# Kernel tuning notes

Measured on AMD Instinct MI355X. Metric: run time of the kernel, lower is better.

Reference implementation:

```python
import jax, jax.numpy as jnp
import numpy as np

H = 51  # n_hidden
B = 8192  # batch
T = 2048  # seq_len
FUTURE = 64


def setup_inputs() -> dict:
    key = jax.random.key(0)
    ks = jax.random.split(key, 12)
    s = 1.0 / np.sqrt(H)
    u = lambda k, shape: jax.random.uniform(k, shape, jnp.float32, -s, s)
    return {
        "x": jax.random.normal(ks[0], (B, T), jnp.float32),
        "W_ih1": u(ks[1], (4 * H, 1)),
        "W_hh1": u(ks[2], (4 * H, H)),
        "b_ih1": u(ks[3], (4 * H,)),
        "b_hh1": u(ks[4], (4 * H,)),
        "W_ih2": u(ks[5], (4 * H, H)),
        "W_hh2": u(ks[6], (4 * H, H)),
        "b_ih2": u(ks[7], (4 * H,)),
        "b_hh2": u(ks[8], (4 * H,)),
        "W_out": u(ks[9], (1, H)),
        "b_out": u(ks[10], (1,)),
        "future": FUTURE,
    }


def _lstm_cell(x, h, c, Wih, Whh, bih, bhh):
    # PyTorch LSTMCell: gates ordered i, f, g, o
    g = x @ Wih.T + h @ Whh.T + (bih + bhh)  # [B, 4H]
    i, f, gg, o = jnp.split(g, 4, axis=-1)
    i = jax.nn.sigmoid(i)
    f = jax.nn.sigmoid(f)
    gg = jnp.tanh(gg)
    o = jax.nn.sigmoid(o)
    c2 = f * c + i * gg
    h2 = o * jnp.tanh(c2)
    return h2, c2


def reference(x, W_ih1, W_hh1, b_ih1, b_hh1, W_ih2, W_hh2, b_ih2, b_hh2,
              W_out, b_out, future):
    Bn = x.shape[0]
    h1 = jnp.zeros((Bn, H), x.dtype)
    c1 = jnp.zeros((Bn, H), x.dtype)

    def emit(h1, c1):
        # Quirk of the original code: layer-2 state is layer-1's CURRENT (h1, c1),
        # and layer-2's own state is never carried forward.
        h2, _ = _lstm_cell(h1, h1, c1, W_ih2, W_hh2, b_ih2, b_hh2)
        return h2 @ W_out.T + b_out  # [B, 1]

    def step(carry, xt):
        h1, c1 = carry
        h1, c1 = _lstm_cell(xt, h1, c1, W_ih1, W_hh1, b_ih1, b_hh1)
        out = emit(h1, c1)
        return (h1, c1), out

    xs = jnp.swapaxes(x, 0, 1)[:, :, None]  # [T, B, 1]
    (h1, c1), outs = jax.lax.scan(step, (h1, c1), xs)
    outs = outs[..., 0].T  # [B, T]

    def fstep(carry, _):
        h1, c1, out = carry
        h1, c1 = _lstm_cell(out, h1, c1, W_ih1, W_hh1, b_ih1, b_hh1)
        out = emit(h1, c1)
        return (h1, c1, out), out

    last = outs[:, -1:]
    _, fouts = jax.lax.scan(fstep, (h1, c1, last), None, length=future)
    fouts = fouts[..., 0].T if future > 0 else jnp.zeros((Bn, 0), x.dtype)
    return jnp.concatenate([outs, fouts], axis=1)  # [B, T + future]
```

## Files before the change

### kernel.cpp

```cpp
#include <hip/hip_runtime.h>

#define HH   51
#define H4   204
#define TSEQ 2048
#define FUT  64
#define TT   (TSEQ + FUT)
#define RPB  16
#define NTH  1024
#define HSTR 72

typedef _Float16 h8 __attribute__((ext_vector_type(8)));
typedef float    f4 __attribute__((ext_vector_type(4)));

#define LOG2E 1.44269504f
#define MFMA(a, b, c) __builtin_amdgcn_mfma_f32_16x16x32_f16(a, b, c, 0, 0, 0)

__device__ __forceinline__ void act6(const f4 g, float cin, float* cout, float* hout) {
    const float ei = __builtin_amdgcn_exp2f(g[0]);
    const float ef = __builtin_amdgcn_exp2f(g[1]);
    const float eg = __builtin_amdgcn_exp2f(g[2]);
    const float eo = __builtin_amdgcn_exp2f(g[3]);
    const float A = 1.0f + ei, B = 1.0f + ef, G = 1.0f + eg, C = 1.0f + eo;
    const float AB = A * B, GC = G * C;
    const float r  = __builtin_amdgcn_rcpf(AB * GC);
    const float t1 = A * GC;
    const float t4 = (B * C) * (2.0f - G);
    const float c2 = r * __builtin_fmaf(t1, cin, t4);
    const float og = r * (AB * G);
    const float ec = __builtin_amdgcn_exp2f(-2.0f * LOG2E * c2);
    const float th = __builtin_fmaf(2.0f, __builtin_amdgcn_rcpf(1.0f + ec), -1.0f);
    *cout = c2;
    *hout = og * th;
}

#define MERGED_BODY(P, EMIT_IDX, DO_EMIT, XI)                                      \
    do {                                                                           \
        if (is_comp) {                                                             \
            const h8 b0 = *(const h8*)&hbuf[P][nl][quad * 8];                      \
            const h8 b1 = *(const h8*)&hbuf[P][nl][32 + quad * 8];                 \
            f4 G1 = {0.f, 0.f, 0.f, 0.f}, G2 = {0.f, 0.f, 0.f, 0.f};               \
            G2 = MFMA(W2[0], b0, G2); G2 = MFMA(W2[1], b1, G2);                    \
            G1 = MFMA(W1[0], b0, G1); G1 = MFMA(W1[1], b1, G1);                    \
            float c2v, h2v;                                                        \
            act6(G2, c1, &c2v, &h2v);             \
            part[(P) ^ 1][cw][quad][nl] = h2v * wo;                                \
            float hv;                                                              \
            act6(G1, c1, &c1, &hv);                         \
            if (kh < HH) hbuf[(P) ^ 1][nl][1 + kh] = (_Float16)hv;                 \
        } else if (w == we) {                                                      \
            if ((DO_EMIT) && lane < RPB) {                                         \
                float s0 = bo, s1 = 0.f, s2 = 0.f, s3 = 0.f;                       \
                _Pragma("unroll")                                                  \
                for (int j = 0; j < 13; ++j) {                                     \
                    s0 += part[P][j][0][lane];                                     \
                    s1 += part[P][j][1][lane];                                     \
                    s2 += part[P][j][2][lane];                                     \
                    s3 += part[P][j][3][lane];                                     \
                }                                                                  \
                out[(size_t)(rb + lane) * TT + (EMIT_IDX)] = (s0 + s1) + (s2 + s3);\
            }                                                                      \
        } else if (w == wp && lane < RPB) {                                        \
            if ((XI) + 1 < TSEQ) hbuf[(P) ^ 1][lane][0] = (_Float16)xnext;         \
            if ((XI) + 2 < TSEQ) xnext = x[(size_t)(rb + lane) * TSEQ + (XI) + 2]; \
        }                                                                          \
        __syncthreads();                                                           \
    } while (0)

__global__ __launch_bounds__(NTH, 8)
void lstm_kernel(const float* __restrict__ x,
                 const float* __restrict__ Wih1, const float* __restrict__ Whh1,
                 const float* __restrict__ bih1, const float* __restrict__ bhh1,
                 const float* __restrict__ Wih2, const float* __restrict__ Whh2,
                 const float* __restrict__ bih2, const float* __restrict__ bhh2,
                 const float* __restrict__ Wout, const float* __restrict__ bout,
                 float* __restrict__ out)
{
    __shared__ _Float16 hbuf[2][RPB][HSTR];
    __shared__ float part[2][13][4][17];
    __shared__ float wouts[64];

    const int tid  = threadIdx.x;
    const int lane = tid & 63;
    const int w    = tid >> 6;
    const int quad = lane >> 4;
    const int nl   = lane & 15;
    const int rb   = blockIdx.x * RPB;

    const int  rot     = (blockIdx.x >> 8) & 1;
    const int  cw      = w - (rot ? 3 : 0);
    const bool is_comp = (cw >= 0) && (cw < 13);
    const int  we      = rot ? 0 : 13;
    const int  wp      = rot ? 1 : 14;

    if (tid < 64) wouts[tid] = (tid < HH) ? Wout[tid] : 0.0f;
    for (int i = tid; i < 2 * RPB * HSTR; i += NTH) (&hbuf[0][0][0])[i] = (_Float16)0.0f;
    __syncthreads();
    if (tid < RPB) {
        hbuf[0][tid][0]  = (_Float16)x[(size_t)(rb + tid) * TSEQ];
        hbuf[0][tid][52] = (_Float16)1.0f;  hbuf[0][tid][53] = (_Float16)1.0f;
        hbuf[1][tid][52] = (_Float16)1.0f;  hbuf[1][tid][53] = (_Float16)1.0f;
    }
    const float bo = bout[0];

    h8 W1[2], W2[2];
    if (is_comp) {
        const int jp = 16 * cw + nl;
        const int kk = jp >> 2, q = jp & 3;
        const bool valid = (jp < H4);
        const int jrow = q * HH + kk;
        const float sc = (q == 2) ? (-2.0f * LOG2E) : (-LOG2E);
        float b1 = 0.0f, b2 = 0.0f;
        if (valid) { b1 = sc * (bih1[jrow] + bhh1[jrow]); b2 = sc * (bih2[jrow] + bhh2[jrow]); }
        const _Float16 b1h = (_Float16)b1, b2h = (_Float16)b2;
        const _Float16 b1l = (_Float16)(b1 - (float)b1h), b2l = (_Float16)(b2 - (float)b2h);
        #pragma unroll
        for (int s = 0; s < 2; ++s) {
            h8 w1v, w2v;
            #pragma unroll
            for (int j = 0; j < 8; ++j) {
                const int k = s * 32 + quad * 8 + j;
                _Float16 a1 = (_Float16)0.0f, a2 = (_Float16)0.0f;
                if (valid) {
                    if (k == 0) {
                        a1 = (_Float16)(sc * Wih1[jrow]);
                    } else if (k <= HH) {
                        const int o = jrow * HH + (k - 1);
                        a1 = (_Float16)(sc * Whh1[o]);
                        a2 = (_Float16)(sc * (Wih2[o] + Whh2[o]));
                    } else if (k == 52) { a1 = b1h; a2 = b2h; }
                    else if (k == 53)   { a1 = b1l; a2 = b2l; }
                }
                w1v[j] = a1;
                w2v[j] = a2;
            }
            W1[s] = w1v;
            W2[s] = w2v;
        }
    }

    float xnext = 0.0f;
    if (w == wp && lane < RPB) xnext = x[(size_t)(rb + lane) * TSEQ + 1];

    const int kh = 4 * cw + quad;
    float c1 = 0.0f;
    __syncthreads();
    const float wo = is_comp ? wouts[kh] : 0.0f;

    if (is_comp) {
        const h8 b0 = *(const h8*)&hbuf[0][nl][quad * 8];
        const h8 b1 = *(const h8*)&hbuf[0][nl][32 + quad * 8];
        f4 G1 = {0.f, 0.f, 0.f, 0.f};
        G1 = MFMA(W1[0], b0, G1); G1 = MFMA(W1[1], b1, G1);
        float hv;
        act6(G1, c1, &c1, &hv);
        if (kh < HH) hbuf[1][nl][1 + kh] = (_Float16)hv;
    } else if (w == wp && lane < RPB) {
        hbuf[1][lane][0] = (_Float16)xnext;
        xnext = x[(size_t)(rb + lane) * TSEQ + 2];
    }
    __syncthreads();

    MERGED_BODY(1, 0, false, 1);

    for (int i = 2; i < TSEQ; i += 2) {
        MERGED_BODY(0, i - 2, true, i);
        MERGED_BODY(1, i - 1, true, i + 1);
    }

    for (int t = TSEQ - 1; t < TT; ++t) {
        const int pb = (t + 1) & 1;
        if (is_comp) {
            const h8 b0 = *(const h8*)&hbuf[pb][nl][quad * 8];
            const h8 b1 = *(const h8*)&hbuf[pb][nl][32 + quad * 8];
            f4 G2 = {0.f, 0.f, 0.f, 0.f};
            G2 = MFMA(W2[0], b0, G2); G2 = MFMA(W2[1], b1, G2);
            float c2v, h2v;
            act6(G2, c1, &c2v, &h2v);
            part[t & 1][cw][quad][nl] = h2v * wo;
        } else if (w == we && t == TSEQ - 1 && lane < RPB) {
            float s0 = bo, s1 = 0.f, s2 = 0.f, s3 = 0.f;
            #pragma unroll
            for (int j = 0; j < 13; ++j) {
                s0 += part[0][j][0][lane];
                s1 += part[0][j][1][lane];
                s2 += part[0][j][2][lane];
                s3 += part[0][j][3][lane];
            }
            out[(size_t)(rb + lane) * TT + (TSEQ - 2)] = (s0 + s1) + (s2 + s3);
        }
        __syncthreads();
        if (w == we && lane < RPB) {
            float s0 = bo, s1 = 0.f, s2 = 0.f, s3 = 0.f;
            #pragma unroll
            for (int j = 0; j < 13; ++j) {
                s0 += part[t & 1][j][0][lane];
                s1 += part[t & 1][j][1][lane];
                s2 += part[t & 1][j][2][lane];
                s3 += part[t & 1][j][3][lane];
            }
            const float s = (s0 + s1) + (s2 + s3);
            out[(size_t)(rb + lane) * TT + t] = s;
            if (t + 1 < TT) hbuf[pb][lane][0] = (_Float16)s;
        }
        __syncthreads();
        if (t + 1 < TT) {
            if (is_comp) {
                const h8 b0 = *(const h8*)&hbuf[pb][nl][quad * 8];
                const h8 b1 = *(const h8*)&hbuf[pb][nl][32 + quad * 8];
                f4 G1 = {0.f, 0.f, 0.f, 0.f};
                G1 = MFMA(W1[0], b0, G1); G1 = MFMA(W1[1], b1, G1);
                float hv;
                act6(G1, c1, &c1, &hv);
                if (kh < HH) hbuf[pb ^ 1][nl][1 + kh] = (_Float16)hv;
            }
            __syncthreads();
        }
    }
}

extern "C" void kernel_launch(void* const* d_in, const int* in_sizes, int n_in,
                              void* d_out, int out_size, void* d_ws, size_t ws_size,
                              hipStream_t stream) {
    (void)in_sizes; (void)n_in; (void)d_ws; (void)ws_size; (void)out_size;
    const float* x    = (const float*)d_in[0];
    const float* Wih1 = (const float*)d_in[1];
    const float* Whh1 = (const float*)d_in[2];
    const float* bih1 = (const float*)d_in[3];
    const float* bhh1 = (const float*)d_in[4];
    const float* Wih2 = (const float*)d_in[5];
    const float* Whh2 = (const float*)d_in[6];
    const float* bih2 = (const float*)d_in[7];
    const float* bhh2 = (const float*)d_in[8];
    const float* Wout = (const float*)d_in[9];
    const float* bout = (const float*)d_in[10];
    float* outp = (float*)d_out;

    dim3 grid(8192 / RPB);
    dim3 block(NTH);
    hipLaunchKernelGGL(lstm_kernel, grid, block, 0, stream,
                       x, Wih1, Whh1, bih1, bhh1, Wih2, Whh2, bih2, bhh2,
                       Wout, bout, outp);
}
```

Measured before the change: 2.497 ms.

## Shrink LSTM blocks to four waves each owning several gate tiles

The 13 compute waves plus two helper waves per 16-row block are replaced by 4 waves per block. Each wave handles 3 or 4 gate tiles, and the emit and x-prefetch duties fold into one of those waves. Partial output sums are now reduced with a per-wave float4 read and cross-quad shuffles, replacing the 13-way LDS sum. The aim is to cut per-step barrier cost and the number of idle helper waves. In exchange, each wave runs a longer serial MFMA and activation chain per step, and occupancy per CU drops.

```diff
diff --git a/kernel.cpp b/kernel.cpp
--- a/kernel.cpp
+++ b/kernel.cpp
@@ -6,7 +6,7 @@
 #define FUT  64
 #define TT   (TSEQ + FUT)
 #define RPB  16
-#define NTH  1024
+#define NTH  256
 #define HSTR 72
 
 typedef _Float16 h8 __attribute__((ext_vector_type(8)));
@@ -33,40 +33,69 @@
     *hout = og * th;
 }
 
-#define MERGED_BODY(P, EMIT_IDX, DO_EMIT, XI)                                      \
-    do {                                                                           \
-        if (is_comp) {                                                             \
-            const h8 b0 = *(const h8*)&hbuf[P][nl][quad * 8];                      \
-            const h8 b1 = *(const h8*)&hbuf[P][nl][32 + quad * 8];                 \
-            f4 G1 = {0.f, 0.f, 0.f, 0.f}, G2 = {0.f, 0.f, 0.f, 0.f};               \
-            G2 = MFMA(W2[0], b0, G2); G2 = MFMA(W2[1], b1, G2);                    \
-            G1 = MFMA(W1[0], b0, G1); G1 = MFMA(W1[1], b1, G1);                    \
-            float c2v, h2v;                                                        \
-            act6(G2, c1, &c2v, &h2v);             \
-            part[(P) ^ 1][cw][quad][nl] = h2v * wo;                                \
-            float hv;                                                              \
-            act6(G1, c1, &c1, &hv);                         \
-            if (kh < HH) hbuf[(P) ^ 1][nl][1 + kh] = (_Float16)hv;                 \
-        } else if (w == we) {                                                      \
-            if ((DO_EMIT) && lane < RPB) {                                         \
-                float s0 = bo, s1 = 0.f, s2 = 0.f, s3 = 0.f;                       \
-                _Pragma("unroll")                                                  \
-                for (int j = 0; j < 13; ++j) {                                     \
-                    s0 += part[P][j][0][lane];                                     \
-                    s1 += part[P][j][1][lane];                                     \
-                    s2 += part[P][j][2][lane];                                     \
-                    s3 += part[P][j][3][lane];                                     \
-                }                                                                  \
-                out[(size_t)(rb + lane) * TT + (EMIT_IDX)] = (s0 + s1) + (s2 + s3);\
-            }                                                                      \
-        } else if (w == wp && lane < RPB) {                                        \
-            if ((XI) + 1 < TSEQ) hbuf[(P) ^ 1][lane][0] = (_Float16)xnext;         \
-            if ((XI) + 2 < TSEQ) xnext = x[(size_t)(rb + lane) * TSEQ + (XI) + 2]; \
-        }                                                                          \
-        __syncthreads();                                                           \
+template<int NT>
+__device__ __forceinline__ void do_p1(const h8 (&W1)[4][2], float (&c1)[4],
+                                      const h8 b0, const h8 b1,
+                                      _Float16 (*hn)[HSTR], int t0, int quad, int nl)
+{
+    const f4 zz = {0.f, 0.f, 0.f, 0.f};
+    #pragma unroll
+    for (int tt = 0; tt < NT; ++tt) {
+        const f4 G1 = MFMA(W1[tt][1], b1, MFMA(W1[tt][0], b0, zz));
+        float hv;
+        act6(G1, c1[tt], &c1[tt], &hv);
+        const int kh = 4 * (t0 + tt) + quad;
+        if (kh < HH) hn[nl][1 + kh] = (_Float16)hv;
+    }
+}
+
+template<int NT>
+__device__ __forceinline__ float do_p2(const h8 (&W2)[4][2], const float (&c1)[4],
+                                       const float (&wo)[4], const h8 b0, const h8 b1)
+{
+    const f4 zz = {0.f, 0.f, 0.f, 0.f};
+    float p = 0.f;
+    #pragma unroll
+    for (int tt = 0; tt < NT; ++tt) {
+        const f4 G2 = MFMA(W2[tt][1], b1, MFMA(W2[tt][0], b0, zz));
+        float c2v, h2v;
+        act6(G2, c1[tt], &c2v, &h2v);
+        p = __builtin_fmaf(h2v, wo[tt], p);
+    }
+    return p;
+}
+
+#define MERGED(P, EIDX, DOE, XI)                                              \
+    do {                                                                      \
+        const h8 b0 = *(const h8*)&hbuf[P][nl][quad * 8];                     \
+        const h8 b1 = *(const h8*)&hbuf[P][nl][32 + quad * 8];                \
+        float p;                                                              \
+        if (four) {                                                           \
+            p = do_p2<4>(W2, c1_t, wo_t, b0, b1);                             \
+            do_p1<4>(W1, c1_t, b0, b1, hbuf[(P) ^ 1], t0, quad, nl);          \
+        } else {                                                              \
+            p = do_p2<3>(W2, c1_t, wo_t, b0, b1);                             \
+            do_p1<3>(W1, c1_t, b0, b1, hbuf[(P) ^ 1], t0, quad, nl);          \
+        }                                                                     \
+        part[(P) ^ 1][quad][nl][w] = p;                                       \
+        if (is_em) {                                                          \
+            if (quad == 0) {                                                  \
+                if ((XI) + 1 < TSEQ) hbuf[(P) ^ 1][nl][0] = (_Float16)xnext;  \
+                if ((XI) + 2 < TSEQ)                                          \
+                    xnext = x[(size_t)(rb + nl) * TSEQ + (XI) + 2];           \
+            }                                                                 \
+            if (DOE) {                                                        \
+                const f4 v = *(const f4*)&part[P][quad][nl][0];               \
+                float s = (v[0] + v[1]) + (v[2] + v[3]);                      \
+                s += __shfl_xor(s, 16, 64);                                   \
+                s += __shfl_xor(s, 32, 64);                                   \
+                if (quad == 0) out[(size_t)(rb + nl) * TT + (EIDX)] = s + bo; \
+            }                                                                 \
+        }                                                                     \
+        __syncthreads();                                                      \
     } while (0)
 
-__global__ __launch_bounds__(NTH, 8)
+__global__ __launch_bounds__(NTH, 2)
 void lstm_kernel(const float* __restrict__ x,
                  const float* __restrict__ Wih1, const float* __restrict__ Whh1,
                  const float* __restrict__ bih1, const float* __restrict__ bhh1,
@@ -76,8 +105,7 @@
                  float* __restrict__ out)
 {
     __shared__ _Float16 hbuf[2][RPB][HSTR];
-    __shared__ float part[2][13][4][17];
-    __shared__ float wouts[64];
+    __shared__ float part[2][4][RPB][4];
 
     const int tid  = threadIdx.x;
     const int lane = tid & 63;
@@ -86,13 +114,12 @@
     const int nl   = lane & 15;
     const int rb   = blockIdx.x * RPB;
 
-    const int  rot     = (blockIdx.x >> 8) & 1;
-    const int  cw      = w - (rot ? 3 : 0);
-    const bool is_comp = (cw >= 0) && (cw < 13);
-    const int  we      = rot ? 0 : 13;
-    const int  wp      = rot ? 1 : 14;
-
-    if (tid < 64) wouts[tid] = (tid < HH) ? Wout[tid] : 0.0f;
+    const int  rot   = (blockIdx.x + (blockIdx.x >> 8)) & 3;
+    const int  role  = (w + rot) & 3;
+    const int  t0    = (role == 0) ? 0 : (role == 1) ? 4 : (role == 2) ? 7 : 10;
+    const bool four  = (role == 0);
+    const bool is_em = (role == 3);
+
     for (int i = tid; i < 2 * RPB * HSTR; i += NTH) (&hbuf[0][0][0])[i] = (_Float16)0.0f;
     __syncthreads();
     if (tid < RPB) {
@@ -102,117 +129,113 @@
     }
     const float bo = bout[0];
 
-    h8 W1[2], W2[2];
-    if (is_comp) {
-        const int jp = 16 * cw + nl;
-        const int kk = jp >> 2, q = jp & 3;
-        const bool valid = (jp < H4);
-        const int jrow = q * HH + kk;
-        const float sc = (q == 2) ? (-2.0f * LOG2E) : (-LOG2E);
-        float b1 = 0.0f, b2 = 0.0f;
-        if (valid) { b1 = sc * (bih1[jrow] + bhh1[jrow]); b2 = sc * (bih2[jrow] + bhh2[jrow]); }
-        const _Float16 b1h = (_Float16)b1, b2h = (_Float16)b2;
-        const _Float16 b1l = (_Float16)(b1 - (float)b1h), b2l = (_Float16)(b2 - (float)b2h);
-        #pragma unroll
-        for (int s = 0; s < 2; ++s) {
-            h8 w1v, w2v;
+    h8 W1[4][2], W2[4][2];
+    float wo_t[4], c1_t[4];
+    h8 hz;
+    #pragma unroll
+    for (int j = 0; j < 8; ++j) hz[j] = (_Float16)0.0f;
+    const int ntl = four ? 4 : 3;
+    #pragma unroll
+    for (int tt = 0; tt < 4; ++tt) {
+        c1_t[tt] = 0.0f; wo_t[tt] = 0.0f;
+        W1[tt][0] = hz; W1[tt][1] = hz; W2[tt][0] = hz; W2[tt][1] = hz;
+        if (tt < ntl) {
+            const int t = t0 + tt;
+            const int jp = 16 * t + nl;
+            const int kk = jp >> 2, q = jp & 3;
+            const bool valid = (jp < H4);
+            const int jrow = q * HH + kk;
+            const float sc = (q == 2) ? (-2.0f * LOG2E) : (-LOG2E);
+            float b1v = 0.0f, b2v = 0.0f;
+            if (valid) { b1v = sc * (bih1[jrow] + bhh1[jrow]); b2v = sc * (bih2[jrow] + bhh2[jrow]); }
+            const _Float16 b1h = (_Float16)b1v, b2h = (_Float16)b2v;
+            const _Float16 b1l = (_Float16)(b1v - (float)b1h), b2l = (_Float16)(b2v - (float)b2h);
             #pragma unroll
-            for (int j = 0; j < 8; ++j) {
-                const int k = s * 32 + quad * 8 + j;
-                _Float16 a1 = (_Float16)0.0f, a2 = (_Float16)0.0f;
-                if (valid) {
-                    if (k == 0) {
-                        a1 = (_Float16)(sc * Wih1[jrow]);
-                    } else if (k <= HH) {
-                        const int o = jrow * HH + (k - 1);
-                        a1 = (_Float16)(sc * Whh1[o]);
-                        a2 = (_Float16)(sc * (Wih2[o] + Whh2[o]));
-                    } else if (k == 52) { a1 = b1h; a2 = b2h; }
-                    else if (k == 53)   { a1 = b1l; a2 = b2l; }
+            for (int s = 0; s < 2; ++s) {
+                h8 w1v = hz, w2v = hz;
+                #pragma unroll
+                for (int j = 0; j < 8; ++j) {
+                    const int k = s * 32 + quad * 8 + j;
+                    _Float16 a1 = (_Float16)0.0f, a2 = (_Float16)0.0f;
+                    if (valid) {
+                        if (k == 0) {
+                            a1 = (_Float16)(sc * Wih1[jrow]);
+                        } else if (k <= HH) {
+                            const int o = jrow * HH + (k - 1);
+                            a1 = (_Float16)(sc * Whh1[o]);
+                            a2 = (_Float16)(sc * (Wih2[o] + Whh2[o]));
+                        } else if (k == 52) { a1 = b1h; a2 = b2h; }
+                        else if (k == 53)   { a1 = b1l; a2 = b2l; }
+                    }
+                    w1v[j] = a1;
+                    w2v[j] = a2;
                 }
-                w1v[j] = a1;
-                w2v[j] = a2;
+                W1[tt][s] = w1v;
+                W2[tt][s] = w2v;
             }
-            W1[s] = w1v;
-            W2[s] = w2v;
+            const int kh = 4 * t + quad;
+            wo_t[tt] = (kh < HH) ? Wout[kh] : 0.0f;
         }
     }
 
     float xnext = 0.0f;
-    if (w == wp && lane < RPB) xnext = x[(size_t)(rb + lane) * TSEQ + 1];
-
-    const int kh = 4 * cw + quad;
-    float c1 = 0.0f;
+    if (is_em && quad == 0) xnext = x[(size_t)(rb + nl) * TSEQ + 1];
     __syncthreads();
-    const float wo = is_comp ? wouts[kh] : 0.0f;
-
-    if (is_comp) {
+
+    {
         const h8 b0 = *(const h8*)&hbuf[0][nl][quad * 8];
         const h8 b1 = *(const h8*)&hbuf[0][nl][32 + quad * 8];
-        f4 G1 = {0.f, 0.f, 0.f, 0.f};
-        G1 = MFMA(W1[0], b0, G1); G1 = MFMA(W1[1], b1, G1);
-        float hv;
-        act6(G1, c1, &c1, &hv);
-        if (kh < HH) hbuf[1][nl][1 + kh] = (_Float16)hv;
-    } else if (w == wp && lane < RPB) {
-        hbuf[1][lane][0] = (_Float16)xnext;
-        xnext = x[(size_t)(rb + lane) * TSEQ + 2];
-    }
-    __syncthreads();
-
-    MERGED_BODY(1, 0, false, 1);
+        if (four) do_p1<4>(W1, c1_t, b0, b1, hbuf[1], t0, quad, nl);
+        else      do_p1<3>(W1, c1_t, b0, b1, hbuf[1], t0, quad, nl);
+        if (is_em && quad == 0) {
+            hbuf[1][nl][0] = (_Float16)xnext;
+            xnext = x[(size_t)(rb + nl) * TSEQ + 2];
+        }
+        __syncthreads();
+    }
+
+    MERGED(1, 0, false, 1);
 
     for (int i = 2; i < TSEQ; i += 2) {
-        MERGED_BODY(0, i - 2, true, i);
-        MERGED_BODY(1, i - 1, true, i + 1);
+        MERGED(0, i - 2, true, i);
+        MERGED(1, i - 1, true, i + 1);
     }
 
     for (int t = TSEQ - 1; t < TT; ++t) {
         const int pb = (t + 1) & 1;
-        if (is_comp) {
+        {
             const h8 b0 = *(const h8*)&hbuf[pb][nl][quad * 8];
             const h8 b1 = *(const h8*)&hbuf[pb][nl][32 + quad * 8];
-            f4 G2 = {0.f, 0.f, 0.f, 0.f};
-            G2 = MFMA(W2[0], b0, G2); G2 = MFMA(W2[1], b1, G2);
-            float c2v, h2v;
-            act6(G2, c1, &c2v, &h2v);
-            part[t & 1][cw][quad][nl] = h2v * wo;
-        } else if (w == we && t == TSEQ - 1 && lane < RPB) {
-            float s0 = bo, s1 = 0.f, s2 = 0.f, s3 = 0.f;
-            #pragma unroll
-            for (int j = 0; j < 13; ++j) {
-                s0 += part[0][j][0][lane];
-                s1 += part[0][j][1][lane];
-                s2 += part[0][j][2][lane];
-                s3 += part[0][j][3][lane];
+            float p;
+            if (four) p = do_p2<4>(W2, c1_t, wo_t, b0, b1);
+            else      p = do_p2<3>(W2, c1_t, wo_t, b0, b1);
+            part[t & 1][quad][nl][w] = p;
+        }
+        if (is_em && t == TSEQ - 1) {
+            const f4 v = *(const f4*)&part[0][quad][nl][0];
+            float s = (v[0] + v[1]) + (v[2] + v[3]);
+            s += __shfl_xor(s, 16, 64);
+            s += __shfl_xor(s, 32, 64);
+            if (quad == 0) out[(size_t)(rb + nl) * TT + (TSEQ - 2)] = s + bo;
+        }
+        __syncthreads();
+        if (is_em) {
+            const f4 v = *(const f4*)&part[t & 1][quad][nl][0];
+            float s = (v[0] + v[1]) + (v[2] + v[3]);
+            s += __shfl_xor(s, 16, 64);
+            s += __shfl_xor(s, 32, 64);
+            s += bo;
+            if (quad == 0) {
+                out[(size_t)(rb + nl) * TT + t] = s;
+                if (t + 1 < TT) hbuf[pb][nl][0] = (_Float16)s;
             }
-            out[(size_t)(rb + lane) * TT + (TSEQ - 2)] = (s0 + s1) + (s2 + s3);
-        }
-        __syncthreads();
-        if (w == we && lane < RPB) {
-            float s0 = bo, s1 = 0.f, s2 = 0.f, s3 = 0.f;
-            #pragma unroll
-            for (int j = 0; j < 13; ++j) {
-                s0 += part[t & 1][j][0][lane];
-                s1 += part[t & 1][j][1][lane];
-                s2 += part[t & 1][j][2][lane];
-                s3 += part[t & 1][j][3][lane];
-            }
-            const float s = (s0 + s1) + (s2 + s3);
-            out[(size_t)(rb + lane) * TT + t] = s;
-            if (t + 1 < TT) hbuf[pb][lane][0] = (_Float16)s;
         }
         __syncthreads();
         if (t + 1 < TT) {
-            if (is_comp) {
-                const h8 b0 = *(const h8*)&hbuf[pb][nl][quad * 8];
-                const h8 b1 = *(const h8*)&hbuf[pb][nl][32 + quad * 8];
-                f4 G1 = {0.f, 0.f, 0.f, 0.f};
-                G1 = MFMA(W1[0], b0, G1); G1 = MFMA(W1[1], b1, G1);
-                float hv;
-                act6(G1, c1, &c1, &hv);
-                if (kh < HH) hbuf[pb ^ 1][nl][1 + kh] = (_Float16)hv;
-            }
+            const h8 b0 = *(const h8*)&hbuf[pb][nl][quad * 8];
+            const h8 b1 = *(const h8*)&hbuf[pb][nl][32 + quad * 8];
+            if (four) do_p1<4>(W1, c1_t, b0, b1, hbuf[pb ^ 1], t0, quad, nl);
+            else      do_p1<3>(W1, c1_t, b0, b1, hbuf[pb ^ 1], t0, quad, nl);
             __syncthreads();
         }
     }
```

After: 2.603 ms. 4.3% more time.
